# Kernel optimization log

Measured on AMD Instinct MI355X. Metric: run time of the kernel, lower is better.

The kernel has to match this reference:

```python
import jax, jax.numpy as jnp
import numpy as np

B, D, H, C = 512, 1024, 512, 4


def setup_inputs() -> dict:
    key = jax.random.key(0)
    k_x, k_v, k_w = jax.random.split(key, 3)
    # x holds categorical values in [0, C) used as float multipliers
    x = jax.random.randint(k_x, (B, D), 0, C).astype(jnp.float32)
    # xavier_normal_ per torch fan computation: V fan_in=D*C, fan_out=H*C; W fan_in=D, fan_out=H
    V = jax.random.normal(k_v, (H, D, C), jnp.float32) * np.float32(np.sqrt(2.0 / (D * C + H * C)))
    b = jnp.zeros((D, C), jnp.float32)
    W = jax.random.normal(k_w, (H, D), jnp.float32) * np.float32(np.sqrt(2.0 / (D + H)))
    c = jnp.zeros((1, H), jnp.float32)
    return {"x": x, "V": V, "b": b, "W": W, "c": c}


def _nade_forward(x, V, b, W, c):
    Bsz = x.shape[0]
    a0 = jnp.broadcast_to(c, (Bsz, c.shape[1]))  # [B, H]
    # per-step slices stacked along leading D axis for lax.scan
    xs = (jnp.transpose(V, (1, 0, 2)),  # [D, H, C]
          b,                            # [D, C]
          W.T,                          # [D, H]
          x.T)                          # [D, B]

    def step(a, inp):
        V_d, b_d, w_d, x_d = inp
        h = jax.nn.sigmoid(a)                 # [B, H]
        logits = h @ V_d + b_d                # [B, C]
        p = jax.nn.log_softmax(logits, axis=1)
        a_new = a + x_d[:, None] * w_d[None, :]  # rank-1 update of running preactivation
        return a_new, (logits, p)

    _, (logits, p) = jax.lax.scan(step, a0, xs)   # each [D, B, C]
    y_hat = jnp.transpose(logits, (1, 0, 2)).reshape(Bsz, -1)  # [B, D*C], d-major blocks of size C
    p_hat = jnp.transpose(p, (1, 0, 2)).reshape(Bsz, -1)
    return y_hat, p_hat


def reference(x, V, b, W, c):
    return _nade_forward(x, V, b, W, c)
```

## Files before the change

### kernel.cpp

```cpp
#include <hip/hip_runtime.h>


#define Bv 512
#define Dv 1024
#define Hv 512
#define Cv 4
#define Kv 32
#define DCv 32

#define L2E 1.4426950408889634f
#define LN2 0.6931471805599453f

typedef __attribute__((ext_vector_type(8))) short short8;
typedef __attribute__((ext_vector_type(4))) float f32x4;

__device__ __forceinline__ float fexp2(float x) { return __builtin_amdgcn_exp2f(x); }
__device__ __forceinline__ float flog2(float x) { return __builtin_amdgcn_logf(x); }
__device__ __forceinline__ float frcp(float x)  { return __builtin_amdgcn_rcpf(x); }

__device__ __forceinline__ unsigned bf16pk(float lo, float hi) {
    return __builtin_amdgcn_perm(__float_as_uint(hi), __float_as_uint(lo), 0x07060302u);
}
__device__ __forceinline__ unsigned short bf16rne(float f) {
    unsigned u = __float_as_uint(f);
    return (unsigned short)((u + 0x7FFFu + ((u >> 16) & 1u)) >> 16);
}

__global__ __launch_bounds__(256) void k_prepW(const float* __restrict__ W,
                                               float* __restrict__ WtL) {
    __shared__ float t[64][65];
    const int tile = blockIdx.x;
    const int tr   = tile >> 4;
    const int tc   = tile & 15;
    const int lx = threadIdx.x & 15;
    const int ly = threadIdx.x >> 4;
#pragma unroll
    for (int r = 0; r < 64; r += 16) {
        int row = r + ly;
        float4 v = *(const float4*)(W + (size_t)(tr * 64 + row) * Dv + tc * 64 + lx * 4);
        t[row][lx * 4 + 0] = v.x;
        t[row][lx * 4 + 1] = v.y;
        t[row][lx * 4 + 2] = v.z;
        t[row][lx * 4 + 3] = v.w;
    }
    __syncthreads();
#pragma unroll
    for (int r = 0; r < 64; r += 16) {
        int row = r + ly;
        float4 o = make_float4(t[lx * 4 + 0][row] * L2E,
                               t[lx * 4 + 1][row] * L2E,
                               t[lx * 4 + 2][row] * L2E,
                               t[lx * 4 + 3][row] * L2E);
        *(float4*)(WtL + (size_t)(tc * 64 + row) * 512 + tr * 64 + lx * 4) = o;
    }
}

__global__ __launch_bounds__(512) void k_mid(
        const float* __restrict__ x, const float* __restrict__ V,
        const float* __restrict__ WtL,
        unsigned short* __restrict__ VtA4, float* __restrict__ xt,
        float* __restrict__ A0) {
    __shared__ __align__(16) char smem[16640];
    const int blk = blockIdx.x;

    if (blk < 2048) {
        float* xs = (float*)smem;
        const int k  = blk >> 6;
        const int bg = blk & 63;
        const int h  = threadIdx.x;
        const int d0 = k * DCv;
        if (threadIdx.x < DCv * 8) {
            int g = threadIdx.x >> 5;
            int j = threadIdx.x & 31;
            xs[j * 8 + g] = x[(size_t)(bg * 8 + g) * Dv + d0 + j];
        }
        __syncthreads();
        float acc[8];
#pragma unroll
        for (int g = 0; g < 8; ++g) acc[g] = 0.0f;
        const float* wp = WtL + (size_t)d0 * Hv + h;
        for (int j = 0; j < DCv; ++j) {
            float wv = wp[(size_t)j * Hv];
            const float4 x0 = *(const float4*)(xs + j * 8);
            const float4 x1 = *(const float4*)(xs + j * 8 + 4);
            acc[0] = fmaf(x0.x, wv, acc[0]);
            acc[1] = fmaf(x0.y, wv, acc[1]);
            acc[2] = fmaf(x0.z, wv, acc[2]);
            acc[3] = fmaf(x0.w, wv, acc[3]);
            acc[4] = fmaf(x1.x, wv, acc[4]);
            acc[5] = fmaf(x1.y, wv, acc[5]);
            acc[6] = fmaf(x1.z, wv, acc[6]);
            acc[7] = fmaf(x1.w, wv, acc[7]);
        }
#pragma unroll
        for (int g = 0; g < 8; ++g)
            A0[((size_t)k * Bv + bg * 8 + g) * Hv + h] = acc[g];
    } else if (blk < 2304) {
        unsigned short* tile = (unsigned short*)smem;
        const int d0  = (blk - 2048) * 4;
        const int dd  = threadIdx.x & 3;
        const int hb0 = threadIdx.x >> 2;
#pragma unroll
        for (int p = 0; p < 4; ++p) {
            int h = p * 128 + hb0;
            float4 v = *(const float4*)(V + ((size_t)h * Dv + d0 + dd) * Cv);
            int hb = h >> 5, q = (h >> 3) & 3, j = h & 7;
            int base = ((dd * 16 + hb) * 16 + q * 4) * 8 + j;
            tile[base + 0 * 8] = bf16rne(v.x);
            tile[base + 1 * 8] = bf16rne(v.y);
            tile[base + 2 * 8] = bf16rne(v.z);
            tile[base + 3 * 8] = bf16rne(v.w);
        }
        __syncthreads();
        uint4* dst = (uint4*)(VtA4 + (size_t)d0 * 2048);
        const uint4* srcp = (const uint4*)tile;
        for (int tt = threadIdx.x; tt < 1024; tt += 512) dst[tt] = srcp[tt];
    } else {
        float (*t)[65] = (float(*)[65])smem;
        const int tile = blk - 2304;
        const int tr   = tile >> 4;
        const int tc   = tile & 15;
        const int lx = threadIdx.x & 15;
        const int ly = threadIdx.x >> 4;
#pragma unroll
        for (int r = 0; r < 64; r += 32) {
            int row = r + ly;
            float4 v = *(const float4*)(x + (size_t)(tr * 64 + row) * Dv + tc * 64 + lx * 4);
            t[row][lx * 4 + 0] = v.x;
            t[row][lx * 4 + 1] = v.y;
            t[row][lx * 4 + 2] = v.z;
            t[row][lx * 4 + 3] = v.w;
        }
        __syncthreads();
#pragma unroll
        for (int r = 0; r < 64; r += 32) {
            int row = r + ly;
            float4 o = make_float4(t[lx * 4 + 0][row],
                                   t[lx * 4 + 1][row],
                                   t[lx * 4 + 2][row],
                                   t[lx * 4 + 3][row]);
            *(float4*)(xt + (size_t)(tc * 64 + row) * 512 + tr * 64 + lx * 4) = o;
        }
    }
}

__global__ void k_prefix(float* __restrict__ A0, const float* __restrict__ cbias) {
    int gid = blockIdx.x * blockDim.x + threadIdx.x;
    int h = gid & (Hv - 1);
    int bi = gid >> 9;
    float run = cbias[h] * L2E;
    float* p = A0 + (size_t)bi * Hv + h;
    for (int k = 0; k < Kv; ++k) {
        float t = p[(size_t)k * Bv * Hv];
        p[(size_t)k * Bv * Hv] = run;
        run += t;
    }
}

__global__ __launch_bounds__(256, 4) void k_main(
        const float* __restrict__ xt, const float* __restrict__ bbias,
        const unsigned short* __restrict__ VtA4, const float* __restrict__ WtL,
        const float* __restrict__ A0, float* __restrict__ out) {
    const int k    = blockIdx.x >> 5;
    const int bg   = blockIdx.x & 31;
    const int wid  = threadIdx.x >> 6;
    const int lane = threadIdx.x & 63;
    const int bl   = lane & 15;
    const int quad = lane >> 4;
    const int b    = bg * 16 + bl;
    const int d0   = k * DCv;
    const int stp  = wid >> 1;
    const bool isP = wid & 1;

    __shared__ f32x4 red[2][2][4][64];

    float a[32];
    {
        const float* ap = A0 + ((size_t)k * Bv + b) * Hv + wid * 128 + quad * 8;
#pragma unroll
        for (int kb = 0; kb < 4; ++kb) {
            float4 t0 = *(const float4*)(ap + kb * 32);
            float4 t1 = *(const float4*)(ap + kb * 32 + 4);
            a[kb*8+0]=t0.x; a[kb*8+1]=t0.y; a[kb*8+2]=t0.z; a[kb*8+3]=t0.w;
            a[kb*8+4]=t1.x; a[kb*8+5]=t1.y; a[kb*8+6]=t1.z; a[kb*8+7]=t1.w;
        }
    }

    const bool act = (bl < 4);
    const unsigned short* vp = VtA4 + (((size_t)d0 * 16 + wid * 4) * 16 + quad * 4 + bl) * 8;
    const float* wp = WtL + (size_t)d0 * Hv + wid * 128 + quad * 8;
    const float* xp = xt + (size_t)d0 * Bv + b;
    const float* bp = bbias + (d0 + stp) * Cv;
    float* sp = out + (isP ? (size_t)Bv * Dv * Cv : (size_t)0)
                    + (size_t)b * Dv * Cv + (d0 + stp) * Cv;

    const short8 zfrag = {0,0,0,0,0,0,0,0};

    for (int i1 = 0; i1 < DCv / 2; ++i1) {
        short8 afA[4], afB[4];
#pragma unroll
        for (int kb = 0; kb < 4; ++kb)
            afA[kb] = act ? *(const short8*)(vp + kb * 128) : zfrag;
#pragma unroll
        for (int kb = 0; kb < 4; ++kb)
            afB[kb] = act ? *(const short8*)(vp + 2048 + kb * 128) : zfrag;
        float xdA = xp[0];
        float xdB = xp[Bv];
        float4 bbv = *(const float4*)bp;

        unsigned pkA[16];
#pragma unroll
        for (int m = 0; m < 32; m += 2) {
            float s0 = frcp(1.0f + fexp2(-a[m]));
            float s1 = frcp(1.0f + fexp2(-a[m + 1]));
            pkA[m >> 1] = bf16pk(s0, s1);
        }
        f32x4 accA = {0.f, 0.f, 0.f, 0.f};
#pragma unroll
        for (int kb = 0; kb < 4; ++kb) {
            union { unsigned u[4]; short8 s; } cv;
            cv.u[0] = pkA[kb*4+0]; cv.u[1] = pkA[kb*4+1];
            cv.u[2] = pkA[kb*4+2]; cv.u[3] = pkA[kb*4+3];
            accA = __builtin_amdgcn_mfma_f32_16x16x32_bf16(afA[kb], cv.s, accA, 0, 0, 0);
        }
#pragma unroll
        for (int kb = 0; kb < 4; ++kb)
#pragma unroll
            for (int j = 0; j < 8; ++j)
                a[kb*8+j] = fmaf(xdA, wp[kb*32+j], a[kb*8+j]);

        unsigned pkB[16];
#pragma unroll
        for (int m = 0; m < 32; m += 2) {
            float s0 = frcp(1.0f + fexp2(-a[m]));
            float s1 = frcp(1.0f + fexp2(-a[m + 1]));
            pkB[m >> 1] = bf16pk(s0, s1);
        }
        f32x4 accB = {0.f, 0.f, 0.f, 0.f};
#pragma unroll
        for (int kb = 0; kb < 4; ++kb) {
            union { unsigned u[4]; short8 s; } cv;
            cv.u[0] = pkB[kb*4+0]; cv.u[1] = pkB[kb*4+1];
            cv.u[2] = pkB[kb*4+2]; cv.u[3] = pkB[kb*4+3];
            accB = __builtin_amdgcn_mfma_f32_16x16x32_bf16(afB[kb], cv.s, accB, 0, 0, 0);
        }
#pragma unroll
        for (int kb = 0; kb < 4; ++kb)
#pragma unroll
            for (int j = 0; j < 8; ++j)
                a[kb*8+j] = fmaf(xdB, wp[Hv + kb*32+j], a[kb*8+j]);

        red[i1 & 1][0][wid][lane] = accA;
        red[i1 & 1][1][wid][lane] = accB;
        __syncthreads();

        f32x4 r0 = red[i1 & 1][stp][0][lane];
        f32x4 r1 = red[i1 & 1][stp][1][lane];
        f32x4 r2 = red[i1 & 1][stp][2][lane];
        f32x4 r3 = red[i1 & 1][stp][3][lane];
        float w0 = r0.x + r1.x + r2.x + r3.x + bbv.x;
        float w1 = r0.y + r1.y + r2.y + r3.y + bbv.y;
        float w2 = r0.z + r1.z + r2.z + r3.z + bbv.z;
        float w3 = r0.w + r1.w + r2.w + r3.w + bbv.w;

        if (!isP) {
            if (quad == 0) *(float4*)sp = make_float4(w0, w1, w2, w3);
        } else {
            float mx = fmaxf(fmaxf(w0, w1), fmaxf(w2, w3));
            float e0 = fexp2((w0 - mx) * L2E);
            float e1 = fexp2((w1 - mx) * L2E);
            float e2 = fexp2((w2 - mx) * L2E);
            float e3 = fexp2((w3 - mx) * L2E);
            float lse = mx + flog2(e0 + e1 + e2 + e3) * LN2;
            if (quad == 0)
                *(float4*)sp = make_float4(w0 - lse, w1 - lse, w2 - lse, w3 - lse);
        }

        vp += 2 * 2048;
        wp += 2 * Hv;
        xp += 2 * Bv;
        bp += 2 * Cv;
        sp += 2 * Cv;
    }
}

extern "C" void kernel_launch(void* const* d_in, const int* in_sizes, int n_in,
                              void* d_out, int out_size, void* d_ws, size_t ws_size,
                              hipStream_t stream) {
    const float* x  = (const float*)d_in[0];
    const float* V  = (const float*)d_in[1];
    const float* bb = (const float*)d_in[2];
    const float* W  = (const float*)d_in[3];
    const float* cb = (const float*)d_in[4];
    float* out = (float*)d_out;

    char* ws = (char*)d_ws;
    unsigned short* VtA4 = (unsigned short*)ws;
    float* WtL = (float*)(ws + (size_t)4 * 1024 * 1024);
    float* xt  = (float*)(ws + (size_t)6 * 1024 * 1024);
    float* A0  = (float*)(ws + (size_t)8 * 1024 * 1024);

    k_prepW<<<128, 256, 0, stream>>>(W, WtL);
    k_mid<<<2432, 512, 0, stream>>>(x, V, WtL, VtA4, xt, A0);
    k_prefix<<<(Bv * Hv) / 256, 256, 0, stream>>>(A0, cb);
    k_main<<<Kv * 32, 256, 0, stream>>>(xt, bb, VtA4, WtL, A0, out);
}
```

Measured before the change: 167.6 us.

## Fold W transpose into k_mid and reorder A0 layout to batch-major

Removes the separate k_prepW launch by adding W-transpose blocks to k_mid. The A0 partial-sum blocks now read W directly (strided by row, scaled by log2e inline) instead of depending on the pre-transposed WtL. A0 is also re-laid out as [B][K][H], so the prefix kernel walks contiguous rows. This saves one launch and its dependency, but W reads in the A0 blocks are now strided per thread and less coalesced.

```diff
diff --git a/kernel.cpp b/kernel.cpp
--- a/kernel.cpp
+++ b/kernel.cpp
@@ -26,40 +26,11 @@
     return (unsigned short)((u + 0x7FFFu + ((u >> 16) & 1u)) >> 16);
 }
 
-__global__ __launch_bounds__(256) void k_prepW(const float* __restrict__ W,
-                                               float* __restrict__ WtL) {
-    __shared__ float t[64][65];
-    const int tile = blockIdx.x;
-    const int tr   = tile >> 4;
-    const int tc   = tile & 15;
-    const int lx = threadIdx.x & 15;
-    const int ly = threadIdx.x >> 4;
-#pragma unroll
-    for (int r = 0; r < 64; r += 16) {
-        int row = r + ly;
-        float4 v = *(const float4*)(W + (size_t)(tr * 64 + row) * Dv + tc * 64 + lx * 4);
-        t[row][lx * 4 + 0] = v.x;
-        t[row][lx * 4 + 1] = v.y;
-        t[row][lx * 4 + 2] = v.z;
-        t[row][lx * 4 + 3] = v.w;
-    }
-    __syncthreads();
-#pragma unroll
-    for (int r = 0; r < 64; r += 16) {
-        int row = r + ly;
-        float4 o = make_float4(t[lx * 4 + 0][row] * L2E,
-                               t[lx * 4 + 1][row] * L2E,
-                               t[lx * 4 + 2][row] * L2E,
-                               t[lx * 4 + 3][row] * L2E);
-        *(float4*)(WtL + (size_t)(tc * 64 + row) * 512 + tr * 64 + lx * 4) = o;
-    }
-}
-
 __global__ __launch_bounds__(512) void k_mid(
         const float* __restrict__ x, const float* __restrict__ V,
-        const float* __restrict__ WtL,
-        unsigned short* __restrict__ VtA4, float* __restrict__ xt,
-        float* __restrict__ A0) {
+        const float* __restrict__ W,
+        unsigned short* __restrict__ VtA4, float* __restrict__ WtL,
+        float* __restrict__ xt, float* __restrict__ A0) {
     __shared__ __align__(16) char smem[16640];
     const int blk = blockIdx.x;
 
@@ -78,9 +49,9 @@
         float acc[8];
 #pragma unroll
         for (int g = 0; g < 8; ++g) acc[g] = 0.0f;
-        const float* wp = WtL + (size_t)d0 * Hv + h;
+        const float* wr = W + (size_t)h * Dv + d0;
         for (int j = 0; j < DCv; ++j) {
-            float wv = wp[(size_t)j * Hv];
+            float wv = wr[j] * L2E;
             const float4 x0 = *(const float4*)(xs + j * 8);
             const float4 x1 = *(const float4*)(xs + j * 8 + 4);
             acc[0] = fmaf(x0.x, wv, acc[0]);
@@ -94,7 +65,7 @@
         }
 #pragma unroll
         for (int g = 0; g < 8; ++g)
-            A0[((size_t)k * Bv + bg * 8 + g) * Hv + h] = acc[g];
+            A0[((size_t)(bg * 8 + g) * Kv + k) * Hv + h] = acc[g];
     } else if (blk < 2304) {
         unsigned short* tile = (unsigned short*)smem;
         const int d0  = (blk - 2048) * 4;
@@ -117,15 +88,20 @@
         for (int tt = threadIdx.x; tt < 1024; tt += 512) dst[tt] = srcp[tt];
     } else {
         float (*t)[65] = (float(*)[65])smem;
-        const int tile = blk - 2304;
+        const int t2   = blk - 2304;
+        const int mb   = t2 >> 7;
+        const int tile = t2 & 127;
         const int tr   = tile >> 4;
         const int tc   = tile & 15;
+        const float* src = mb ? W : x;
+        float* dst       = mb ? WtL : xt;
+        const float scale = mb ? L2E : 1.0f;
         const int lx = threadIdx.x & 15;
         const int ly = threadIdx.x >> 4;
 #pragma unroll
         for (int r = 0; r < 64; r += 32) {
             int row = r + ly;
-            float4 v = *(const float4*)(x + (size_t)(tr * 64 + row) * Dv + tc * 64 + lx * 4);
+            float4 v = *(const float4*)(src + (size_t)(tr * 64 + row) * Dv + tc * 64 + lx * 4);
             t[row][lx * 4 + 0] = v.x;
             t[row][lx * 4 + 1] = v.y;
             t[row][lx * 4 + 2] = v.z;
@@ -135,11 +111,11 @@
 #pragma unroll
         for (int r = 0; r < 64; r += 32) {
             int row = r + ly;
-            float4 o = make_float4(t[lx * 4 + 0][row],
-                                   t[lx * 4 + 1][row],
-                                   t[lx * 4 + 2][row],
-                                   t[lx * 4 + 3][row]);
-            *(float4*)(xt + (size_t)(tc * 64 + row) * 512 + tr * 64 + lx * 4) = o;
+            float4 o = make_float4(t[lx * 4 + 0][row] * scale,
+                                   t[lx * 4 + 1][row] * scale,
+                                   t[lx * 4 + 2][row] * scale,
+                                   t[lx * 4 + 3][row] * scale);
+            *(float4*)(dst + (size_t)(tc * 64 + row) * 512 + tr * 64 + lx * 4) = o;
         }
     }
 }
@@ -149,10 +125,10 @@
     int h = gid & (Hv - 1);
     int bi = gid >> 9;
     float run = cbias[h] * L2E;
-    float* p = A0 + (size_t)bi * Hv + h;
+    float* p = A0 + (size_t)bi * (Kv * Hv) + h;
     for (int k = 0; k < Kv; ++k) {
-        float t = p[(size_t)k * Bv * Hv];
-        p[(size_t)k * Bv * Hv] = run;
+        float t = p[(size_t)k * Hv];
+        p[(size_t)k * Hv] = run;
         run += t;
     }
 }
@@ -176,7 +152,7 @@
 
     float a[32];
     {
-        const float* ap = A0 + ((size_t)k * Bv + b) * Hv + wid * 128 + quad * 8;
+        const float* ap = A0 + ((size_t)b * Kv + k) * Hv + wid * 128 + quad * 8;
 #pragma unroll
         for (int kb = 0; kb < 4; ++kb) {
             float4 t0 = *(const float4*)(ap + kb * 32);
@@ -300,8 +276,7 @@
     float* xt  = (float*)(ws + (size_t)6 * 1024 * 1024);
     float* A0  = (float*)(ws + (size_t)8 * 1024 * 1024);
 
-    k_prepW<<<128, 256, 0, stream>>>(W, WtL);
-    k_mid<<<2432, 512, 0, stream>>>(x, V, WtL, VtA4, xt, A0);
+    k_mid<<<2560, 512, 0, stream>>>(x, V, W, VtA4, WtL, xt, A0);
     k_prefix<<<(Bv * Hv) / 256, 256, 0, stream>>>(A0, cb);
     k_main<<<Kv * 32, 256, 0, stream>>>(xt, bb, VtA4, WtL, A0, out);
 }
```

After: 175.9 us. +5.0%, slower.
